# Kernel optimization log

Measured on AMD Instinct MI355X. Metric: run time of the kernel, lower is better.

The kernel has to match this reference:

```python
import jax, jax.numpy as jnp
import numpy as np
import math

B, L, D, H, VD, AD = 2, 1024, 512, 8, 12, 1
HD = D // H

def _rope(q, k):
    # q, k: (B, H, L, HD). LLaMA-style rotary embedding (theta=10000), interleaved pairs.
    hd = q.shape[-1]
    inv = 1.0 / (10000.0 ** (jnp.arange(0, hd, 2, dtype=jnp.float32) / hd))  # (hd/2,)
    ang = jnp.arange(q.shape[2], dtype=jnp.float32)[:, None] * inv[None, :]  # (L, hd/2)
    cos = jnp.cos(ang)[None, None]  # (1,1,L,hd/2)
    sin = jnp.sin(ang)[None, None]
    def rot(t):
        tr, ti = t[..., 0::2], t[..., 1::2]
        outr = tr * cos - ti * sin
        outi = tr * sin + ti * cos
        return jnp.stack([outr, outi], axis=-1).reshape(t.shape)
    return rot(q), rot(k)

def setup_inputs() -> dict:
    key = jax.random.key(0)
    ks = jax.random.split(key, 24)
    def n(k, shape, scale=1.0):
        return jax.random.normal(k, shape, dtype=jnp.float32) * scale
    sD = 1.0 / math.sqrt(D)
    sV = 1.0 / math.sqrt(3 * H * VD)
    sA = 1.0 / math.sqrt(3 * H * AD)
    return {
        "x": n(ks[0], (B, L, D)),
        "mask": jnp.ones((B, L), dtype=jnp.float32),
        "rots": n(ks[1], (B, L, 3, 3)),
        "trans": n(ks[2], (B, L, 3)),
        "w_q": n(ks[3], (D, D), sD), "w_k": n(ks[4], (D, D), sD),
        "w_v": n(ks[5], (D, D), sD), "w_o": n(ks[6], (D, D), sD),
        "w_vq_w": n(ks[7], (D, 3 * H * VD), sD), "w_vq_b": n(ks[8], (3 * H * VD,), 0.02),
        "w_vk_w": n(ks[9], (D, 3 * H * VD), sD), "w_vk_b": n(ks[10], (3 * H * VD,), 0.02),
        "w_vv_w": n(ks[11], (D, 3 * H * VD), sD), "w_vv_b": n(ks[12], (3 * H * VD,), 0.02),
        "w_vo_w": n(ks[13], (3 * H * VD, D), sV), "w_vo_b": n(ks[14], (D,), 0.02),
        "w_aq_w": n(ks[15], (D, 3 * H * AD), sD), "w_aq_b": n(ks[16], (3 * H * AD,), 0.02),
        "w_av_w": n(ks[17], (D, 3 * H * AD), sD), "w_av_b": n(ks[18], (3 * H * AD,), 0.02),
        "w_ao_w": n(ks[19], (3 * H * AD, D), sA), "w_ao_b": n(ks[20], (D,), 0.02),
        "affine_w": n(ks[21], (H,), 0.5),
    }

def reference(x, mask, rots, trans, w_q, w_k, w_v, w_o,
              w_vq_w, w_vq_b, w_vk_w, w_vk_b, w_vv_w, w_vv_b, w_vo_w, w_vo_b,
              w_aq_w, w_aq_b, w_av_w, w_av_b, w_ao_w, w_ao_b, affine_w):
    Bs, Ls, Dd = x.shape
    INF = 1e6
    # --- scalar attention with RoPE ---
    q = (x @ w_q).reshape(Bs, Ls, H, HD).transpose(0, 2, 1, 3)  # (B,H,L,HD)
    k = (x @ w_k).reshape(Bs, Ls, H, HD).transpose(0, 2, 1, 3)
    q, k = _rope(q, k)
    scalar_attn = jnp.einsum('bhid,bhjd->bhij', q, k) / math.sqrt(Dd)
    # --- rotated-vector attention ---
    def proj_rot(w, b, vd):
        v = (x @ w + b).reshape(Bs, Ls, H, vd, 3)
        # v @ rots.mT  ->  sum_c v[...,c] * R[d,c]
        return jnp.einsum('blhvc,bldc->blhvd', v, rots)
    vq = proj_rot(w_vq_w, w_vq_b, VD).reshape(Bs, Ls, H, 3 * VD).transpose(0, 2, 1, 3)
    vk = proj_rot(w_vk_w, w_vk_b, VD).reshape(Bs, Ls, H, 3 * VD).transpose(0, 2, 1, 3)
    vector_attn = jnp.einsum('bhid,bhjd->bhij', vq, vk) / math.sqrt(3 * VD)
    # --- affine (pairwise point distance) attention; note source uses w_aq for both q and k ---
    aq = proj_rot(w_aq_w, w_aq_b, AD) + trans[:, :, None, None]  # (B,L,H,AD,3)
    aq = aq.transpose(0, 2, 1, 3, 4)                              # (B,H,L,AD,3)
    diff = aq[:, :, :, None] - aq[:, :, None]                     # (B,H,L,L,AD,3)
    affine_attn = -jnp.sqrt(jnp.square(diff).sum(-1)).sum(-1)     # (B,H,L,L)
    affine_attn = jax.nn.softplus(affine_w)[None, :, None, None] * affine_attn
    attn = scalar_attn + vector_attn + affine_attn
    attn = attn - INF * (1.0 - mask[:, None, None, :])
    attn = jax.nn.softmax(attn, axis=-1)
    # --- scalar output ---
    v = (x @ w_v).reshape(Bs, Ls, H, HD).transpose(0, 2, 1, 3)
    scalar_out = jnp.einsum('bhij,bhjd->bhid', attn, v).transpose(0, 2, 1, 3).reshape(Bs, Ls, Dd)
    # --- vector output (aggregate in global frame, rotate back) ---
    vv = proj_rot(w_vv_w, w_vv_b, VD)                             # (B,L,H,VD,3)
    vec = jnp.einsum('bhij,bjhvc->bhivc', attn, vv)               # (B,H,L,VD,3)
    vec = jnp.einsum('bhlvc,blcn->bhlvn', vec, rots)              # @ rots
    vector_out = vec.transpose(0, 2, 1, 3, 4).reshape(Bs, Ls, 3 * H * VD)
    # --- affine output ---
    av = proj_rot(w_av_w, w_av_b, AD) + trans[:, :, None, None]   # (B,L,H,AD,3)
    aff = jnp.einsum('bhij,bjhvc->bhivc', attn, av)               # (B,H,L,AD,3)
    aff = aff - trans[:, None, :, None]                            # subtract (B,1,L,1,3)
    aff = jnp.einsum('bhlvc,blcn->bhlvn', aff, rots)
    affine_out = aff.transpose(0, 2, 1, 3, 4).reshape(Bs, Ls, 3 * H * AD)
    return scalar_out @ w_o + (vector_out @ w_vo_w + w_vo_b) + (affine_out @ w_ao_w + w_ao_b)
```

## Files before the change

### kernel.cpp

```cpp
#include <hip/hip_runtime.h>
#include <math.h>

namespace {

typedef __attribute__((ext_vector_type(8))) short short8;
typedef __attribute__((ext_vector_type(4))) float f32x4;

constexpr int NL  = 1024;
constexpr int ND  = 512;
constexpr int NH  = 8;
constexpr int NV3 = 36;
constexpr int NCAT = 2560;
constexpr int KF   = 832;

constexpr float SCL_S = 0.044194173824159216f;
constexpr float SCL_V = 1.0f / 6.0f;
constexpr float FIXM  = 12.0f;

__device__ inline ushort f2bf(float f) {
  uint u = __float_as_uint(f);
  u += 0x7FFFu + ((u >> 16) & 1u);
  return (ushort)(u >> 16);
}
__device__ inline float bf2f(ushort h) { return __uint_as_float((uint)h << 16); }

#define MFMA(a, b, c) __builtin_amdgcn_mfma_f32_16x16x32_bf16((a), (b), (c), 0, 0, 0)

__global__ __launch_bounds__(256) void k_wprep(
    const float* __restrict__ wq, const float* __restrict__ wk,
    const float* __restrict__ wv, const float* __restrict__ wvq,
    const float* __restrict__ wvk, const float* __restrict__ wvv,
    const float* __restrict__ waq, const float* __restrict__ wav,
    const float* __restrict__ w_o, const float* __restrict__ w_vo,
    const float* __restrict__ w_ao, const float* __restrict__ x,
    ushort* __restrict__ wch, ushort* __restrict__ wcat2,
    ushort* __restrict__ xh, ushort* __restrict__ xl)
{
  __shared__ float t[64][65];
  const int tid = threadIdx.x;
  const int z = blockIdx.z;
  if (z == 2) {
    const int bid = blockIdx.y * 40 + blockIdx.x;
    if (bid >= 512) return;
    const size_t i = ((size_t)bid * 256 + tid) * 8;
#pragma unroll
    for (int q = 0; q < 2; ++q) {
      const float4 v = *(const float4*)&x[i + q * 4];
      ushort4 h, l;
      h.x = f2bf(v.x); l.x = f2bf(v.x - bf2f(h.x));
      h.y = f2bf(v.y); l.y = f2bf(v.y - bf2f(h.y));
      h.z = f2bf(v.z); l.z = f2bf(v.z - bf2f(h.z));
      h.w = f2bf(v.w); l.w = f2bf(v.w - bf2f(h.w));
      *(ushort4*)&xh[i + q * 4] = h;
      *(ushort4*)&xl[i + q * 4] = l;
    }
    return;
  }
  if (z == 0) { if (blockIdx.y >= 8) return; }
  else        { if (blockIdx.x >= 8) return; }
  const int n0 = blockIdx.x * 64, k0 = blockIdx.y * 64;
  const int rr = tid >> 6, cc = tid & 63;

  for (int p = 0; p < 16; ++p) {
    const int kk = k0 + p * 4 + rr;
    const int nn = n0 + cc;
    float val;
    if (z == 0) {
      if (nn < 1536) {
        const float* w = nn < 512 ? wq : (nn < 1024 ? wk : wv);
        val = w[(size_t)kk * 512 + (nn & 511)];
      } else if (nn < 2400) {
        const float* w = nn < 1824 ? wvq : (nn < 2112 ? wvk : wvv);
        val = w[(size_t)kk * 288 + (nn - 1536) % 288];
      } else if (nn < 2424) val = waq[(size_t)kk * 24 + nn - 2400];
      else if (nn < 2448)   val = wav[(size_t)kk * 24 + nn - 2424];
      else val = 0.f;
    } else {
      if (kk < 512)      val = w_o [(size_t)kk * 512 + nn];
      else if (kk < 800) val = w_vo[(size_t)(kk - 512) * 512 + nn];
      else if (kk < 824) val = w_ao[(size_t)(kk - 800) * 512 + nn];
      else val = 0.f;
    }
    t[p * 4 + rr][cc] = val;
  }
  __syncthreads();
  for (int p = 0; p < 16; ++p) {
    const int nn = p * 4 + rr;
    const int kk = cc;
    const float val = t[kk][nn];
    if (z == 0) wch[(size_t)(n0 + nn) * 512 + k0 + kk] = f2bf(val);
    else        wcat2[(size_t)(n0 + nn) * 832 + k0 + kk] = f2bf(val);
  }
}

__global__ __launch_bounds__(256) void k_mm(
    const ushort* __restrict__ Ah, const ushort* __restrict__ Al,
    const ushort* __restrict__ Bh,
    float* __restrict__ Y, int N, int K)
{
  __shared__ __align__(16) ushort Ahs[128][40];
  __shared__ __align__(16) ushort Als[128][40];
  __shared__ __align__(16) ushort Bhs[64][40];
  const int tid = threadIdx.x;
  const int m0 = blockIdx.x * 128, n0 = blockIdx.y * 64;
  const int w = tid >> 6, lane = tid & 63;
  const int wm = (w & 1) * 64, wn = (w >> 1) * 32;
  const int fr = lane & 15, fg = lane >> 4;

  f32x4 acc[4][2];
#pragma unroll
  for (int i = 0; i < 4; ++i)
#pragma unroll
    for (int j = 0; j < 2; ++j) acc[i][j] = (f32x4){0.f, 0.f, 0.f, 0.f};

  const int ar = tid >> 1, ak = (tid & 1) * 16;
  const int br = tid >> 2, bk = (tid & 3) * 8;
  const ushort* agh = Ah + (size_t)(m0 + ar) * K + ak;
  const ushort* agl = Al + (size_t)(m0 + ar) * K + ak;
  const ushort* bgh = Bh + (size_t)(n0 + br) * K + bk;
  short8 pah0 = *(const short8*)agh, pah1 = *(const short8*)(agh + 8);
  short8 pal0 = *(const short8*)agl, pal1 = *(const short8*)(agl + 8);
  short8 pbh0 = *(const short8*)bgh;

  const int NT = K >> 5;
  for (int kt = 0; kt < NT; ++kt) {
    __syncthreads();
    *(short8*)&Ahs[ar][ak] = pah0; *(short8*)&Ahs[ar][ak + 8] = pah1;
    *(short8*)&Als[ar][ak] = pal0; *(short8*)&Als[ar][ak + 8] = pal1;
    *(short8*)&Bhs[br][bk] = pbh0;
    __syncthreads();
    if (kt + 1 < NT) {
      const size_t off = (size_t)(kt + 1) * 32;
      pah0 = *(const short8*)(agh + off); pah1 = *(const short8*)(agh + off + 8);
      pal0 = *(const short8*)(agl + off); pal1 = *(const short8*)(agl + off + 8);
      pbh0 = *(const short8*)(bgh + off);
    }
    short8 fah[4], fal[4], fbh[2];
#pragma unroll
    for (int i = 0; i < 4; ++i) {
      fah[i] = *(const short8*)&Ahs[wm + i * 16 + fr][fg * 8];
      fal[i] = *(const short8*)&Als[wm + i * 16 + fr][fg * 8];
    }
#pragma unroll
    for (int j = 0; j < 2; ++j)
      fbh[j] = *(const short8*)&Bhs[wn + j * 16 + fr][fg * 8];
#pragma unroll
    for (int i = 0; i < 4; ++i)
#pragma unroll
      for (int j = 0; j < 2; ++j) {
        f32x4 t = MFMA(fah[i], fbh[j], acc[i][j]);
        acc[i][j] = MFMA(fal[i], fbh[j], t);
      }
  }

  const int rb = fg * 4;
#pragma unroll
  for (int i = 0; i < 4; ++i)
#pragma unroll
    for (int j = 0; j < 2; ++j) {
      const int n = n0 + wn + j * 16 + fr;
#pragma unroll
      for (int r = 0; r < 4; ++r) {
        const int m = m0 + wm + i * 16 + rb + r;
        Y[(size_t)m * N + n] = acc[i][j][r];
      }
    }
}

__global__ __launch_bounds__(256) void k_fin(
    const ushort* __restrict__ A, const ushort* __restrict__ Bt,
    const float* __restrict__ b_vo, const float* __restrict__ b_ao,
    float* __restrict__ out)
{
  __shared__ __align__(16) ushort As[64][40];
  __shared__ __align__(16) ushort Bs[64][40];
  const int tid = threadIdx.x;
  const int m0 = blockIdx.x * 64, n0 = blockIdx.y * 64;
  const int w = tid >> 6, lane = tid & 63;
  const int wm = (w & 1) * 32, wn = (w >> 1) * 32;
  const int fr = lane & 15, fg = lane >> 4;
  const int K = KF;

  f32x4 acc[2][2];
#pragma unroll
  for (int i = 0; i < 2; ++i)
#pragma unroll
    for (int j = 0; j < 2; ++j) acc[i][j] = (f32x4){0.f, 0.f, 0.f, 0.f};

  const int ar = tid >> 2, ak = (tid & 3) * 8;
  const ushort* ag = A + (size_t)(m0 + ar) * K + ak;
  const ushort* bg = Bt + (size_t)(n0 + ar) * K + ak;
  short8 a0 = *(const short8*)ag;
  short8 b0 = *(const short8*)bg;

  const int NT = K >> 5;
  for (int kt = 0; kt < NT; ++kt) {
    __syncthreads();
    *(short8*)&As[ar][ak] = a0;
    *(short8*)&Bs[ar][ak] = b0;
    __syncthreads();
    if (kt + 1 < NT) {
      const size_t off = (size_t)(kt + 1) * 32;
      a0 = *(const short8*)(ag + off);
      b0 = *(const short8*)(bg + off);
    }
    short8 aF[2], bF[2];
#pragma unroll
    for (int i = 0; i < 2; ++i) aF[i] = *(const short8*)&As[wm + i * 16 + fr][fg * 8];
#pragma unroll
    for (int j = 0; j < 2; ++j) bF[j] = *(const short8*)&Bs[wn + j * 16 + fr][fg * 8];
#pragma unroll
    for (int i = 0; i < 2; ++i)
#pragma unroll
      for (int j = 0; j < 2; ++j)
        acc[i][j] = MFMA(aF[i], bF[j], acc[i][j]);
  }

  const int rb = fg * 4;
#pragma unroll
  for (int j = 0; j < 2; ++j) {
    const int n = n0 + wn + j * 16 + fr;
    const float bias = b_vo[n] + b_ao[n];
#pragma unroll
    for (int i = 0; i < 2; ++i)
#pragma unroll
      for (int r = 0; r < 4; ++r) {
        const int m = m0 + wm + i * 16 + rb + r;
        out[(size_t)m * ND + n] = acc[i][j][r] + bias;
      }
  }
}

__global__ __launch_bounds__(256) void k_stage(
    const float* __restrict__ Y,
    const float* __restrict__ rots, const float* __restrict__ trans,
    const float* __restrict__ mask,
    const float* __restrict__ bvq, const float* __restrict__ bvk,
    const float* __restrict__ bvv, const float* __restrict__ baq,
    const float* __restrict__ bav,
    ushort* __restrict__ qAh, ushort* __restrict__ kBh,
    ushort* __restrict__ Vt,
    float* __restrict__ aq_t, float* __restrict__ penc)
{
  __shared__ __align__(16) char sbuf[36864];
  const int tid = threadIdx.x;

  if (blockIdx.z == 0) {
    float (*t0)[65] = (float(*)[65])sbuf;
    float (*t1)[72] = (float(*)[72])(sbuf + 16640);
    const int l0 = blockIdx.x * 64, h = blockIdx.y;
    const int b = l0 >> 10, ll0 = l0 & 1023;
    const int bh = b * NH + h;
    const int rr = tid >> 6, cc = tid & 63;
    const float inv = powf(10000.f, -(float)(cc & ~1) / 64.f);
    const bool odd = (cc & 1) != 0;

    for (int p = 0; p < 16; ++p) {
      const int r = p * 4 + rr;
      t0[r][cc] = Y[(size_t)(l0 + r) * NCAT + h * 64 + cc];
    }
    __syncthreads();
    for (int p = 0; p < 16; ++p) {
      const int r = p * 4 + rr;
      float sv, cv;
      __sincosf((float)(ll0 + r) * inv, &sv, &cv);
      const float e = t0[r][cc & ~1], o = t0[r][(cc & ~1) + 1];
      const float val = (odd ? fmaf(e, sv, o * cv) : fmaf(e, cv, -o * sv)) * SCL_S;
      qAh[((size_t)bh * NL + ll0 + r) * 128 + cc] = f2bf(val);
    }
    __syncthreads();
    for (int p = 0; p < 16; ++p) {
      const int r = p * 4 + rr;
      t0[r][cc] = Y[(size_t)(l0 + r) * NCAT + 512 + h * 64 + cc];
    }
    __syncthreads();
    for (int p = 0; p < 16; ++p) {
      const int r = p * 4 + rr;
      float sv, cv;
      __sincosf((float)(ll0 + r) * inv, &sv, &cv);
      const float e = t0[r][cc & ~1], o = t0[r][(cc & ~1) + 1];
      const float val = odd ? fmaf(e, sv, o * cv) : fmaf(e, cv, -o * sv);
      kBh[((size_t)bh * NL + ll0 + r) * 128 + cc] = f2bf(val);
    }
    for (int p = 0; p < 16; ++p) {
      const int r = p * 4 + rr;
      t1[cc][r] = Y[(size_t)(l0 + r) * NCAT + 1024 + h * 64 + cc];
    }
    __syncthreads();
    for (int p = 0; p < 16; ++p) {
      const int hd = p * 4 + rr;
      Vt[((size_t)bh * 112 + hd) * NL + ll0 + cc] = f2bf(t1[hd][cc]);
    }
    for (int u = tid; u < 9 * 64; u += 256)
      Vt[((size_t)bh * 112 + 103 + (u >> 6)) * NL + ll0 + (u & 63)] = 0;
    return;
  }

  float (*ys)[912] = (float(*)[912])sbuf;
  const int bid = blockIdx.y * 32 + blockIdx.x;
  const int tb = bid * 8;
  const int b = tb >> 10;

  for (int t = 0; t < 8; ++t)
    for (int n = tid; n < 912; n += 256)
      ys[t][n] = Y[(size_t)(tb + t) * NCAT + 1536 + n];
  __syncthreads();

  for (int u = tid; u < 8 * 288; u += 256) {
    const int t = u / 288, n = u % 288;
    const int l = tb + t, ll = l & (NL - 1);
    const int c = n % 3, base = n - c;
    const int h = n / NV3, m = n % NV3;
    const float r0 = rots[(size_t)l * 9 + c * 3 + 0];
    const float r1 = rots[(size_t)l * 9 + c * 3 + 1];
    const float r2 = rots[(size_t)l * 9 + c * 3 + 2];
    const float vqv = (r0 * (ys[t][base] + bvq[base])
                     + r1 * (ys[t][base + 1] + bvq[base + 1])
                     + r2 * (ys[t][base + 2] + bvq[base + 2])) * SCL_V;
    const float vkv = r0 * (ys[t][288 + base] + bvk[base])
                    + r1 * (ys[t][289 + base] + bvk[base + 1])
                    + r2 * (ys[t][290 + base] + bvk[base + 2]);
    const float vvv = r0 * (ys[t][576 + base] + bvv[base])
                    + r1 * (ys[t][577 + base] + bvv[base + 1])
                    + r2 * (ys[t][578 + base] + bvv[base + 2]);
    const size_t row = ((size_t)(b * NH + h) * NL + ll) * 128 + 64 + m;
    qAh[row] = f2bf(vqv);
    kBh[row] = f2bf(vkv);
    Vt[((size_t)(b * NH + h) * 112 + 64 + m) * NL + ll] = f2bf(vvv);
  }
  for (int u = tid; u < 8 * 8 * 14; u += 256) {
    const int t = u / 112, rem = u % 112, h = rem / 14, k = rem % 14;
    const int ll = (tb + t) & (NL - 1);
    const size_t row = ((size_t)(b * NH + h) * NL + ll) * 128 + 100 + 2 * k;
    *(uint*)&qAh[row] = 0;
  }
  for (int u = tid; u < 64; u += 256) {
    const int t = u >> 3, h = u & 7;
    const int l = tb + t, ll = l & (NL - 1);
    const int base = h * 3;
    const size_t tok = (size_t)(b * NH + h) * NL + ll;
#pragma unroll
    for (int c = 0; c < 3; ++c) {
      const float aqv =
          rots[(size_t)l * 9 + c * 3 + 0] * (ys[t][864 + base] + baq[base])
        + rots[(size_t)l * 9 + c * 3 + 1] * (ys[t][865 + base] + baq[base + 1])
        + rots[(size_t)l * 9 + c * 3 + 2] * (ys[t][866 + base] + baq[base + 2])
        + trans[(size_t)l * 3 + c];
      aq_t[((size_t)(b * NH + h) * 3 + c) * NL + ll] = aqv;
    }
#pragma unroll
    for (int k = 0; k < 14; ++k)
      *(uint*)&kBh[tok * 128 + 100 + 2 * k] = 0;
  }
  for (int u = tid; u < 8 * 24; u += 256) {
    const int t = u / 24, n = u % 24;
    const int l = tb + t, ll = l & (NL - 1);
    const int c = n % 3, h = n / 3, base = h * 3;
    const float val = rots[(size_t)l * 9 + c * 3 + 0] * (ys[t][888 + base] + bav[base])
                    + rots[(size_t)l * 9 + c * 3 + 1] * (ys[t][889 + base] + bav[base + 1])
                    + rots[(size_t)l * 9 + c * 3 + 2] * (ys[t][890 + base] + bav[base + 2])
                    + trans[(size_t)l * 3 + c];
    Vt[((size_t)(b * NH + h) * 112 + 100 + c) * NL + ll] = f2bf(val);
  }
  for (int u = tid; u < 8; u += 256) {
    const int ll = (tb + u) & (NL - 1);
    penc[(size_t)b * NL + ll] = 1e6f * (1.0f - mask[(size_t)b * NL + ll]);
  }
}

__global__ __launch_bounds__(256) void k_attn(
    const ushort* __restrict__ qAh,
    const ushort* __restrict__ kBh, const ushort* __restrict__ Vt,
    const float* __restrict__ aq_t, const float* __restrict__ penc,
    const float* __restrict__ rots, const float* __restrict__ trans,
    const float* __restrict__ affw,
    ushort* __restrict__ catb)
{
  __shared__ __align__(16) ushort Ks[64][136];
  __shared__ __align__(16) ushort Vs[112][72];
  __shared__ float Aqs[4][64];
  __shared__ __align__(16) ushort P_s[4][16][72];
  __shared__ float Ow[4][16][116];

  const int blk = blockIdx.x;
  const int bh  = (blk & 7) * 2 + (blk >> 7);
  const int i0  = ((blk >> 3) & 15) * 64;
  const int b = bh >> 3, h = bh & 7;
  const int tid = threadIdx.x;
  const int w = tid >> 6, lane = tid & 63;
  const int fr = lane & 15, fg = lane >> 4;
  const int irow = i0 + w * 16;

  const float spw = logf(1.0f + expf(affw[h]));

  short8 aQ[4];
  const size_t qrow = ((size_t)bh * NL + irow + fr) * 128;
#pragma unroll
  for (int ks = 0; ks < 4; ++ks)
    aQ[ks] = *(const short8*)&qAh[qrow + ks * 32 + fg * 8];

  const float* aqx = aq_t + (size_t)bh * 3 * NL;
  float ai0[4], ai1[4], ai2[4];
#pragma unroll
  for (int r_ = 0; r_ < 4; ++r_) {
    const int row = irow + fg * 4 + r_;
    ai0[r_] = aqx[row];
    ai1[r_] = aqx[NL + row];
    ai2[r_] = aqx[2 * NL + row];
  }

  float lsum[4] = {0.f, 0.f, 0.f, 0.f};
  f32x4 accO[7];
#pragma unroll
  for (int ct = 0; ct < 7; ++ct) accO[ct] = (f32x4){0.f, 0.f, 0.f, 0.f};

  const int krow = tid >> 2, kc0 = (tid & 3) * 32;
  const int vrow = tid >> 1, vc0 = (tid & 1) * 32;
  const int au = tid - 224;
  const size_t kgb = (size_t)bh * NL * 128 + (size_t)krow * 128 + kc0;
  const size_t vgb = ((size_t)bh * 112 + vrow) * NL + vc0;

  short8 kp[4], vp[4];
  float ap[8];

  auto loadTile = [&](int j0) {
#pragma unroll
    for (int k = 0; k < 4; ++k)
      kp[k] = *(const short8*)&kBh[kgb + (size_t)j0 * 128 + k * 8];
    if (tid < 224) {
#pragma unroll
      for (int k = 0; k < 4; ++k)
        vp[k] = *(const short8*)&Vt[vgb + j0 + k * 8];
    } else {
#pragma unroll
      for (int q = 0; q < 8; ++q) {
        const int idx = au * 8 + q;
        const int c = idx >> 6, jj = idx & 63;
        ap[q] = (c < 3) ? aqx[c * NL + j0 + jj]
                        : penc[(size_t)b * NL + j0 + jj];
      }
    }
  };
  auto storeTile = [&]() {
#pragma unroll
    for (int k = 0; k < 4; ++k)
      *(short8*)&Ks[krow][kc0 + k * 8] = kp[k];
    if (tid < 224) {
#pragma unroll
      for (int k = 0; k < 4; ++k)
        *(short8*)&Vs[vrow][vc0 + k * 8] = vp[k];
    } else {
#pragma unroll
      for (int q = 0; q < 8; ++q) {
        const int idx = au * 8 + q;
        Aqs[idx >> 6][idx & 63] = ap[q];
      }
    }
  };

  loadTile(0);
  for (int t = 0; t < 16; ++t) {
    __syncthreads();
    storeTile();
    __syncthreads();
    if (t < 15) loadTile((t + 1) * 64);

    f32x4 accS[4];
#pragma unroll
    for (int ct = 0; ct < 4; ++ct) accS[ct] = (f32x4){0.f, 0.f, 0.f, 0.f};
#pragma unroll
    for (int ct = 0; ct < 4; ++ct) {
#pragma unroll
      for (int ks = 0; ks < 4; ++ks) {
        const short8 bh8 = *(const short8*)&Ks[ct * 16 + fr][ks * 32 + fg * 8];
        accS[ct] = MFMA(aQ[ks], bh8, accS[ct]);
      }
    }

#pragma unroll
    for (int ct = 0; ct < 4; ++ct) {
      const int jj = ct * 16 + fr;
      const float aj0 = Aqs[0][jj];
      const float aj1 = Aqs[1][jj];
      const float aj2v = Aqs[2][jj];
      const float pen = Aqs[3][jj];
#pragma unroll
      for (int r_ = 0; r_ < 4; ++r_) {
        const float dx = ai0[r_] - aj0;
        const float dy = ai1[r_] - aj1;
        const float dz = ai2[r_] - aj2v;
        const float s = accS[ct][r_]
                      - spw * sqrtf(dx * dx + dy * dy + dz * dz) - pen;
        const float p = __expf(s - FIXM);
        accS[ct][r_] = p;
        lsum[r_] += p;
      }
    }

#pragma unroll
    for (int ct = 0; ct < 4; ++ct)
#pragma unroll
      for (int r_ = 0; r_ < 4; ++r_)
        P_s[w][fg * 4 + r_][ct * 16 + fr] = f2bf(accS[ct][r_]);

    const short8 aP0 = *(const short8*)&P_s[w][fr][fg * 8];
    const short8 aP1 = *(const short8*)&P_s[w][fr][32 + fg * 8];
#pragma unroll
    for (int ct = 0; ct < 7; ++ct) {
      const short8 b0 = *(const short8*)&Vs[ct * 16 + fr][fg * 8];
      const short8 b1 = *(const short8*)&Vs[ct * 16 + fr][32 + fg * 8];
      f32x4 tacc = MFMA(aP0, b0, accO[ct]);
      accO[ct] = MFMA(aP1, b1, tacc);
    }
  }

#pragma unroll
  for (int off = 1; off < 16; off <<= 1) {
#pragma unroll
    for (int r_ = 0; r_ < 4; ++r_) lsum[r_] += __shfl_xor(lsum[r_], off);
  }
  float inv[4];
#pragma unroll
  for (int r_ = 0; r_ < 4; ++r_) inv[r_] = 1.0f / lsum[r_];
#pragma unroll
  for (int ct = 0; ct < 7; ++ct)
#pragma unroll
    for (int r_ = 0; r_ < 4; ++r_)
      Ow[w][fg * 4 + r_][ct * 16 + fr] = accO[ct][r_] * inv[r_];

  for (int u = lane; u < 16 * 103; u += 64) {
    const int lr = u / 103, d = u % 103;
    const int gi = irow + lr;
    const size_t gl = (size_t)b * NL + gi;
    const float* O = Ow[w][lr];
    float val;
    int col;
    if (d < 64) {
      val = O[d];
      col = h * 64 + d;
    } else if (d < 100) {
      const int v3 = d - 64;
      const int n = v3 % 3;
      const int base = 64 + v3 - n;
      val = O[base]     * rots[gl * 9 + n]
          + O[base + 1] * rots[gl * 9 + 3 + n]
          + O[base + 2] * rots[gl * 9 + 6 + n];
      col = 512 + h * NV3 + v3;
    } else {
      const int n = d - 100;
      const float c0 = O[100] - trans[gl * 3 + 0];
      const float c1 = O[101] - trans[gl * 3 + 1];
      const float c2 = O[102] - trans[gl * 3 + 2];
      val = c0 * rots[gl * 9 + n] + c1 * rots[gl * 9 + 3 + n] + c2 * rots[gl * 9 + 6 + n];
      col = 800 + h * 3 + n;
    }
    catb[gl * KF + col] = f2bf(val);
  }
  if (h == 0) {
    for (int u = tid; u < 64 * 8; u += 256)
      catb[((size_t)b * NL + i0 + (u >> 3)) * KF + 824 + (u & 7)] = 0;
  }
}

}

extern "C" void kernel_launch(void* const* d_in, const int* in_sizes, int n_in,
                              void* d_out, int out_size, void* d_ws, size_t ws_size,
                              hipStream_t stream)
{
  const float* x       = (const float*)d_in[0];
  const float* mask    = (const float*)d_in[1];
  const float* rots    = (const float*)d_in[2];
  const float* trans   = (const float*)d_in[3];
  const float* w_q     = (const float*)d_in[4];
  const float* w_k     = (const float*)d_in[5];
  const float* w_v     = (const float*)d_in[6];
  const float* w_o     = (const float*)d_in[7];
  const float* w_vq_w  = (const float*)d_in[8];
  const float* w_vq_b  = (const float*)d_in[9];
  const float* w_vk_w  = (const float*)d_in[10];
  const float* w_vk_b  = (const float*)d_in[11];
  const float* w_vv_w  = (const float*)d_in[12];
  const float* w_vv_b  = (const float*)d_in[13];
  const float* w_vo_w  = (const float*)d_in[14];
  const float* w_vo_b  = (const float*)d_in[15];
  const float* w_aq_w  = (const float*)d_in[16];
  const float* w_aq_b  = (const float*)d_in[17];
  const float* w_av_w  = (const float*)d_in[18];
  const float* w_av_b  = (const float*)d_in[19];
  const float* w_ao_w  = (const float*)d_in[20];
  const float* w_ao_b  = (const float*)d_in[21];
  const float* aff_w   = (const float*)d_in[22];
  float* out = (float*)d_out;

  char* base = (char*)d_ws;
  ushort* xh  = (ushort*)base;
  ushort* xl  = xh + (size_t)2048 * 512;
  ushort* wch = xl + (size_t)2048 * 512;
  ushort* qAh = (ushort*)base;
  float*  aq_t = (float*)(wch + (size_t)2560 * 512);
  char* p = base + 9437184;
  ushort* wcat2 = (ushort*)p; p += (size_t)512 * 832 * 2;
  float*  Y     = (float*)p;
  ushort* catb  = (ushort*)Y;
  p += (size_t)2048 * 2560 * 4;
  ushort* kBh = (ushort*)p; p += (size_t)16 * 1024 * 128 * 2;
  ushort* Vt  = (ushort*)p; p += (size_t)16 * 112 * 1024 * 2;
  float* penc = (float*)p;  p += (size_t)2048 * 4;

  k_wprep<<<dim3(40, 13, 3), 256, 0, stream>>>(w_q, w_k, w_v, w_vq_w, w_vk_w,
                                               w_vv_w, w_aq_w, w_av_w,
                                               w_o, w_vo_w, w_ao_w, x,
                                               wch, wcat2, xh, xl);
  k_mm<<<dim3(16, 40), 256, 0, stream>>>(xh, xl, wch, Y, NCAT, 512);
  k_stage<<<dim3(32, 8, 2), 256, 0, stream>>>(Y, rots, trans, mask,
                                              w_vq_b, w_vk_b, w_vv_b,
                                              w_aq_b, w_av_b,
                                              qAh, kBh, Vt, aq_t, penc);
  k_attn<<<256, 256, 0, stream>>>(qAh, kBh, Vt,
                                  aq_t, penc, rots, trans, aff_w, catb);
  k_fin<<<dim3(32, 8), 256, 0, stream>>>(catb, wcat2, w_vo_b, w_ao_b, out);
}
```

Measured before the change: 112.5 us.

## Split attention key range across two wave groups per block

The attention kernel now runs 512 threads per block: two groups of four waves each process one half of the key sequence, so each runs 8 tile iterations instead of 16. Partial outputs and row sums are written to shared memory as bf16 and fp32 and combined before the final normalization and rotation epilogue. The aim is more waves in flight per CU, which matters because the grid has only 256 blocks. In exchange it uses more shared memory and registers per block, and storing the partial outputs in bf16 adds rounding error.

```diff
diff --git a/kernel.cpp b/kernel.cpp
--- a/kernel.cpp
+++ b/kernel.cpp
@@ -368,7 +368,7 @@
   }
 }
 
-__global__ __launch_bounds__(256) void k_attn(
+__global__ __launch_bounds__(512) void k_attn(
     const ushort* __restrict__ qAh,
     const ushort* __restrict__ kBh, const ushort* __restrict__ Vt,
     const float* __restrict__ aq_t, const float* __restrict__ penc,
@@ -376,11 +376,15 @@
     const float* __restrict__ affw,
     ushort* __restrict__ catb)
 {
-  __shared__ __align__(16) ushort Ks[64][136];
-  __shared__ __align__(16) ushort Vs[112][72];
-  __shared__ float Aqs[4][64];
-  __shared__ __align__(16) ushort P_s[4][16][72];
-  __shared__ float Ow[4][16][116];
+  __shared__ __align__(16) ushort Ks[2][64][136];
+  __shared__ __align__(16) ushort Vs[2][112][72];
+  __shared__ float Aqs[2][4][64];
+  __shared__ __align__(16) char uni[28672];
+  __shared__ float lst[8][16];
+  __shared__ float linv[4][16];
+
+  ushort (*P_s)[16][72]   = (ushort(*)[16][72])uni;
+  ushort (*Opart)[16][112] = (ushort(*)[16][112])uni;
 
   const int blk = blockIdx.x;
   const int bh  = (blk & 7) * 2 + (blk >> 7);
@@ -388,8 +392,9 @@
   const int b = bh >> 3, h = bh & 7;
   const int tid = threadIdx.x;
   const int w = tid >> 6, lane = tid & 63;
+  const int rg = w & 3, jh = w >> 2;
   const int fr = lane & 15, fg = lane >> 4;
-  const int irow = i0 + w * 16;
+  const int irow = i0 + rg * 16;
 
   const float spw = logf(1.0f + expf(affw[h]));
 
@@ -414,56 +419,59 @@
 #pragma unroll
   for (int ct = 0; ct < 7; ++ct) accO[ct] = (f32x4){0.f, 0.f, 0.f, 0.f};
 
-  const int krow = tid >> 2, kc0 = (tid & 3) * 32;
-  const int vrow = tid >> 1, vc0 = (tid & 1) * 32;
-  const int au = tid - 224;
-  const size_t kgb = (size_t)bh * NL * 128 + (size_t)krow * 128 + kc0;
-  const size_t vgb = ((size_t)bh * 112 + vrow) * NL + vc0;
+  const int hk = tid >> 8, krow = (tid >> 2) & 63, kc0 = (tid & 3) * 32;
+  const int hv = (tid < 448) ? tid / 224 : 0;
+  const int vrem = (tid < 448) ? tid % 224 : 0;
+  const int vrow = vrem >> 1, vc0 = (vrem & 1) * 32;
+  const int au = tid - 448;
+  const size_t kgb = (size_t)bh * NL * 128 + (size_t)(hk * 512 + krow) * 128 + kc0;
+  const size_t vgb = ((size_t)bh * 112 + vrow) * NL + hv * 512 + vc0;
 
   short8 kp[4], vp[4];
   float ap[8];
 
-  auto loadTile = [&](int j0) {
+  auto loadTile = [&](int t) {
 #pragma unroll
     for (int k = 0; k < 4; ++k)
-      kp[k] = *(const short8*)&kBh[kgb + (size_t)j0 * 128 + k * 8];
-    if (tid < 224) {
+      kp[k] = *(const short8*)&kBh[kgb + (size_t)t * 64 * 128 + k * 8];
+    if (tid < 448) {
 #pragma unroll
       for (int k = 0; k < 4; ++k)
-        vp[k] = *(const short8*)&Vt[vgb + j0 + k * 8];
+        vp[k] = *(const short8*)&Vt[vgb + t * 64 + k * 8];
     } else {
 #pragma unroll
       for (int q = 0; q < 8; ++q) {
         const int idx = au * 8 + q;
-        const int c = idx >> 6, jj = idx & 63;
-        ap[q] = (c < 3) ? aqx[c * NL + j0 + jj]
-                        : penc[(size_t)b * NL + j0 + jj];
+        const int ha = idx >> 8, rem2 = idx & 255;
+        const int c = rem2 >> 6, jj = rem2 & 63;
+        const int j = ha * 512 + t * 64 + jj;
+        ap[q] = (c < 3) ? aqx[c * NL + j] : penc[(size_t)b * NL + j];
       }
     }
   };
   auto storeTile = [&]() {
 #pragma unroll
     for (int k = 0; k < 4; ++k)
-      *(short8*)&Ks[krow][kc0 + k * 8] = kp[k];
-    if (tid < 224) {
+      *(short8*)&Ks[hk][krow][kc0 + k * 8] = kp[k];
+    if (tid < 448) {
 #pragma unroll
       for (int k = 0; k < 4; ++k)
-        *(short8*)&Vs[vrow][vc0 + k * 8] = vp[k];
+        *(short8*)&Vs[hv][vrow][vc0 + k * 8] = vp[k];
     } else {
 #pragma unroll
       for (int q = 0; q < 8; ++q) {
         const int idx = au * 8 + q;
-        Aqs[idx >> 6][idx & 63] = ap[q];
+        Aqs[idx >> 8][(idx & 255) >> 6][idx & 63] = ap[q];
       }
     }
   };
 
   loadTile(0);
-  for (int t = 0; t < 16; ++t) {
+  for (int t = 0; t < 8; ++t) {
     __syncthreads();
     storeTile();
     __syncthreads();
-    if (t < 15) loadTile((t + 1) * 64);
+    if (t < 7) loadTile(t + 1);
 
     f32x4 accS[4];
 #pragma unroll
@@ -472,7 +480,7 @@
     for (int ct = 0; ct < 4; ++ct) {
 #pragma unroll
       for (int ks = 0; ks < 4; ++ks) {
-        const short8 bh8 = *(const short8*)&Ks[ct * 16 + fr][ks * 32 + fg * 8];
+        const short8 bh8 = *(const short8*)&Ks[jh][ct * 16 + fr][ks * 32 + fg * 8];
         accS[ct] = MFMA(aQ[ks], bh8, accS[ct]);
       }
     }
@@ -480,10 +488,10 @@
 #pragma unroll
     for (int ct = 0; ct < 4; ++ct) {
       const int jj = ct * 16 + fr;
-      const float aj0 = Aqs[0][jj];
-      const float aj1 = Aqs[1][jj];
-      const float aj2v = Aqs[2][jj];
-      const float pen = Aqs[3][jj];
+      const float aj0 = Aqs[jh][0][jj];
+      const float aj1 = Aqs[jh][1][jj];
+      const float aj2v = Aqs[jh][2][jj];
+      const float pen = Aqs[jh][3][jj];
 #pragma unroll
       for (int r_ = 0; r_ < 4; ++r_) {
         const float dx = ai0[r_] - aj0;
@@ -507,8 +515,8 @@
     const short8 aP1 = *(const short8*)&P_s[w][fr][32 + fg * 8];
 #pragma unroll
     for (int ct = 0; ct < 7; ++ct) {
-      const short8 b0 = *(const short8*)&Vs[ct * 16 + fr][fg * 8];
-      const short8 b1 = *(const short8*)&Vs[ct * 16 + fr][32 + fg * 8];
+      const short8 b0 = *(const short8*)&Vs[jh][ct * 16 + fr][fg * 8];
+      const short8 b1 = *(const short8*)&Vs[jh][ct * 16 + fr][32 + fg * 8];
       f32x4 tacc = MFMA(aP0, b0, accO[ct]);
       accO[ct] = MFMA(aP1, b1, tacc);
     }
@@ -519,45 +527,59 @@
 #pragma unroll
     for (int r_ = 0; r_ < 4; ++r_) lsum[r_] += __shfl_xor(lsum[r_], off);
   }
-  float inv[4];
-#pragma unroll
-  for (int r_ = 0; r_ < 4; ++r_) inv[r_] = 1.0f / lsum[r_];
+
+  __syncthreads();
+
 #pragma unroll
   for (int ct = 0; ct < 7; ++ct)
 #pragma unroll
     for (int r_ = 0; r_ < 4; ++r_)
-      Ow[w][fg * 4 + r_][ct * 16 + fr] = accO[ct][r_] * inv[r_];
-
-  for (int u = lane; u < 16 * 103; u += 64) {
+      Opart[w][fg * 4 + r_][ct * 16 + fr] = f2bf(accO[ct][r_]);
+  if (fr == 0) {
+#pragma unroll
+    for (int r_ = 0; r_ < 4; ++r_) lst[w][fg * 4 + r_] = lsum[r_];
+  }
+  __syncthreads();
+
+  if (tid < 64) {
+    const int g = tid >> 4, row = tid & 15;
+    linv[g][row] = 1.0f / (lst[g][row] + lst[g + 4][row]);
+  }
+  __syncthreads();
+
+  auto comb = [&](int row, int d) -> float {
+    const int g = row >> 4, r16 = row & 15;
+    return (bf2f(Opart[g][r16][d]) + bf2f(Opart[g + 4][r16][d])) * linv[g][r16];
+  };
+  for (int u = tid; u < 64 * 103; u += 512) {
     const int lr = u / 103, d = u % 103;
-    const int gi = irow + lr;
+    const int gi = i0 + lr;
     const size_t gl = (size_t)b * NL + gi;
-    const float* O = Ow[w][lr];
     float val;
     int col;
     if (d < 64) {
-      val = O[d];
+      val = comb(lr, d);
       col = h * 64 + d;
     } else if (d < 100) {
       const int v3 = d - 64;
       const int n = v3 % 3;
       const int base = 64 + v3 - n;
-      val = O[base]     * rots[gl * 9 + n]
-          + O[base + 1] * rots[gl * 9 + 3 + n]
-          + O[base + 2] * rots[gl * 9 + 6 + n];
+      val = comb(lr, base)     * rots[gl * 9 + n]
+          + comb(lr, base + 1) * rots[gl * 9 + 3 + n]
+          + comb(lr, base + 2) * rots[gl * 9 + 6 + n];
       col = 512 + h * NV3 + v3;
     } else {
       const int n = d - 100;
-      const float c0 = O[100] - trans[gl * 3 + 0];
-      const float c1 = O[101] - trans[gl * 3 + 1];
-      const float c2 = O[102] - trans[gl * 3 + 2];
+      const float c0 = comb(lr, 100) - trans[gl * 3 + 0];
+      const float c1 = comb(lr, 101) - trans[gl * 3 + 1];
+      const float c2 = comb(lr, 102) - trans[gl * 3 + 2];
       val = c0 * rots[gl * 9 + n] + c1 * rots[gl * 9 + 3 + n] + c2 * rots[gl * 9 + 6 + n];
       col = 800 + h * 3 + n;
     }
     catb[gl * KF + col] = f2bf(val);
   }
   if (h == 0) {
-    for (int u = tid; u < 64 * 8; u += 256)
+    for (int u = tid; u < 64 * 8; u += 512)
       catb[((size_t)b * NL + i0 + (u >> 3)) * KF + 824 + (u & 7)] = 0;
   }
 }
@@ -617,7 +639,7 @@
                                               w_vq_b, w_vk_b, w_vv_b,
                                               w_aq_b, w_av_b,
                                               qAh, kBh, Vt, aq_t, penc);
-  k_attn<<<256, 256, 0, stream>>>(qAh, kBh, Vt,
+  k_attn<<<256, 512, 0, stream>>>(qAh, kBh, Vt,
                                   aq_t, penc, rots, trans, aff_w, catb);
   k_fin<<<dim3(32, 8), 256, 0, stream>>>(catb, wcat2, w_vo_b, w_ao_b, out);
 }
```

Measured after the change: 101.9 us. 9.4% less time.
